# Performance work log

Measured on AMD Instinct MI355X. Metric: run time of the kernel, lower is better.

Reference implementation:

```python
import jax, jax.numpy as jnp
import numpy as np

N = 50000   # nodes
E = 800000  # edges (avg degree 16)
G = 256     # graphs in batch
H = 16      # hidden_channels
ADD = 7     # ADD_FEATURES
EPS = 1e-5


def setup_inputs() -> dict:
    key = jax.random.key(0)
    ks = jax.random.split(key, 32)
    inp = {
        "x": jax.random.normal(ks[0], (N, 1), dtype=jnp.float32),
        "edge_index": jax.random.randint(ks[1], (2, E), 0, N),
        "batch": jnp.sort(jax.random.randint(ks[2], (N,), 0, G)),
        "y_extra": jax.random.normal(ks[3], (G, ADD), dtype=jnp.float32),
    }
    k = 4
    conv_dims = [(1, H), (H, 2 * H), (2 * H, 4 * H), (4 * H, 8 * H)]
    for i, (ci, co) in enumerate(conv_dims, 1):
        inp[f"W{i}"] = (jax.random.normal(ks[k], (ci, co), dtype=jnp.float32) / np.float32(np.sqrt(ci))); k += 1
        inp[f"b{i}"] = jnp.zeros((co,), dtype=jnp.float32)
    for i, c in enumerate([H, 2 * H, 4 * H], 1):
        inp[f"g{i}"] = jnp.ones((c,), jnp.float32) + 0.1 * jax.random.normal(ks[k], (c,), dtype=jnp.float32); k += 1
        inp[f"be{i}"] = 0.1 * jax.random.normal(ks[k], (c,), dtype=jnp.float32); k += 1
    mlp_dims = [(8 * H + ADD, 128), (128, 64), (64, 32), (32, 2)]
    for i, (ci, co) in enumerate(mlp_dims, 1):
        inp[f"lw{i}"] = (jax.random.normal(ks[k], (ci, co), dtype=jnp.float32) / np.float32(np.sqrt(ci))); k += 1
        inp[f"lb{i}"] = 0.01 * jax.random.normal(ks[k], (co,), dtype=jnp.float32); k += 1
    return inp


def _gcn_norm(edge_index, n):
    # PyG GCNConv default: add self loops, symmetric deg^{-1/2} normalization.
    loops = jnp.arange(n)
    src = jnp.concatenate([edge_index[0], loops])
    dst = jnp.concatenate([edge_index[1], loops])
    deg = jax.ops.segment_sum(jnp.ones_like(src, dtype=jnp.float32), dst, num_segments=n)
    dis = jnp.where(deg > 0, jax.lax.rsqrt(jnp.maximum(deg, 1.0)), 0.0)
    return src, dst, dis[src] * dis[dst]


def _gcn_conv(x, W, b, src, dst, norm, n):
    h = x @ W                                   # [N, Cout]
    msg = h[src] * norm[:, None]                # [E+N, Cout] gather
    agg = jax.ops.segment_sum(msg, dst, num_segments=n)  # scatter-add
    return agg + b


def _bn(x, gamma, beta):
    # training-mode BatchNorm1d over node dim (biased variance)
    mu = jnp.mean(x, axis=0)
    var = jnp.mean(jnp.square(x - mu), axis=0)
    return gamma * (x - mu) * jax.lax.rsqrt(var + EPS) + beta


def _gelu(x):
    return jax.nn.gelu(x, approximate=False)  # torch F.gelu default = exact erf


def reference(x, edge_index, batch, y_extra,
              W1, b1, W2, b2, W3, b3, W4, b4,
              g1, be1, g2, be2, g3, be3,
              lw1, lb1, lw2, lb2, lw3, lb3, lw4, lb4):
    n = x.shape[0]
    src, dst, norm = _gcn_norm(edge_index, n)
    h = _gelu(_gcn_conv(x, W1, b1, src, dst, norm, n))
    h = _bn(h, g1, be1)
    h = _gelu(_gcn_conv(h, W2, b2, src, dst, norm, n))
    h = _bn(h, g2, be2)
    h = _gelu(_gcn_conv(h, W3, b3, src, dst, norm, n))
    h = _bn(h, g3, be3)
    h = _gelu(_gcn_conv(h, W4, b4, src, dst, norm, n))
    # global mean pool per graph
    sums = jax.ops.segment_sum(h, batch, num_segments=G)
    cnt = jax.ops.segment_sum(jnp.ones((n,), jnp.float32), batch, num_segments=G)
    pooled = sums / jnp.maximum(cnt, 1.0)[:, None]   # [G, 8H]
    z = jnp.concatenate([pooled, y_extra], axis=1)   # [G, 8H+7]
    z = _gelu(z @ lw1 + lb1)
    z = _gelu(z @ lw2 + lb2)
    z = _gelu(z @ lw3 + lb3)
    return jax.nn.sigmoid(z @ lw4 + lb4)             # [G, 2]
```

## Files before the change

### kernel.cpp

```cpp
#include <hip/hip_runtime.h>
#include <math.h>

#define NN 50000
#define EE 800000
#define GG 256
#define NPB 100
#define NBUCK 500
#define EPB 4096
#define NEB 196
#define NB_NODE 196

__device__ __forceinline__ float gelu_f(float v){
    return 0.5f * v * (1.0f + erff(v * 0.70710678118654752f));
}

__global__ __launch_bounds__(256) void k_hist(const int* __restrict__ dst, int* __restrict__ bucket_cnt_p, int e){
    __shared__ int hist[512];
    int t = threadIdx.x;
    int start = blockIdx.x * EPB;
    for (int k = t; k < 512; k += 256) hist[k] = 0;
    __syncthreads();
#pragma unroll
    for (int k = 0; k < EPB / 256; k++){
        int idx = start + k * 256 + t;
        if (idx < e) atomicAdd(&hist[dst[idx] / NPB], 1);
    }
    __syncthreads();
    for (int k = t; k < NBUCK; k += 256){
        int h = hist[k];
        if (h) atomicAdd(&bucket_cnt_p[k * 16], h);
    }
}

__global__ __launch_bounds__(512) void k_bscan(const int* __restrict__ bucket_cnt_p,
                                               int* __restrict__ bucket_off, int* __restrict__ cursor_p){
    __shared__ int s[512];
    int t = threadIdx.x;
    int v = (t < NBUCK) ? bucket_cnt_p[t * 16] : 0;
    s[t] = v;
    __syncthreads();
    for (int off = 1; off < 512; off <<= 1){
        int u = (t >= off) ? s[t - off] : 0;
        __syncthreads();
        s[t] += u;
        __syncthreads();
    }
    if (t < NBUCK){
        int ex = s[t] - v;
        bucket_off[t] = ex;
        cursor_p[t * 16] = ex;
    }
}

__global__ __launch_bounds__(256) void k_scatter(const int* __restrict__ src, const int* __restrict__ dst,
                                                 int* __restrict__ cursor_p, int* __restrict__ ebuf, int e){
    __shared__ int hist[512], base[512];
    int t = threadIdx.x;
    int start = blockIdx.x * EPB;
    for (int k = t; k < 512; k += 256) hist[k] = 0;
    __syncthreads();
    int pk[EPB / 256], bb[EPB / 256];
    int cntl = 0;
#pragma unroll
    for (int k = 0; k < EPB / 256; k++){
        int idx = start + k * 256 + t;
        if (idx < e){
            int s_ = src[idx], d_ = dst[idx];
            int b_ = d_ / NPB;
            pk[cntl] = (s_ << 7) | (d_ - b_ * NPB);
            bb[cntl] = b_;
            atomicAdd(&hist[b_], 1);
            cntl++;
        }
    }
    __syncthreads();
    for (int k = t; k < NBUCK; k += 256){
        int h = hist[k];
        base[k] = h ? atomicAdd(&cursor_p[k * 16], h) : 0;
    }
    __syncthreads();
    for (int k = t; k < 512; k += 256) hist[k] = 0;
    __syncthreads();
    for (int k = 0; k < cntl; k++){
        int b_ = bb[k];
        int pos = base[b_] + atomicAdd(&hist[b_], 1);
        ebuf[pos] = pk[k];
    }
}

__global__ __launch_bounds__(256) void k_build(const int* __restrict__ ebuf,
                                               const int* __restrict__ bucket_cnt_p,
                                               const int* __restrict__ bucket_off,
                                               int* __restrict__ rp, int* __restrict__ col,
                                               float* __restrict__ dis, float* __restrict__ invdis,
                                               float2* __restrict__ xd,
                                               const float* __restrict__ x, int n){
    int b = blockIdx.x;
    int t = threadIdx.x;
    int nbase = b * NPB;
    int eoff = bucket_off[b];
    int ecnt = bucket_cnt_p[b * 16];
    __shared__ int cnt[128], excl[128], cnt2[128], s[128];
    if (t < 128){ cnt[t] = 0; cnt2[t] = 0; }
    __syncthreads();
    for (int j = t; j < ecnt; j += 256)
        atomicAdd(&cnt[ebuf[eoff + j] & 127], 1);
    __syncthreads();
    int v = (t < 128) ? cnt[t] : 0;
    if (t < 128) s[t] = v;
    __syncthreads();
    for (int off = 1; off < 128; off <<= 1){
        int u = (t < 128 && t >= off) ? s[t - off] : 0;
        __syncthreads();
        if (t < 128) s[t] += u;
        __syncthreads();
    }
    if (t < 128) excl[t] = s[t] - v;
    __syncthreads();
    if (t < NPB){
        int node = nbase + t;
        int dgg = cnt[t];
        rp[node] = eoff + excl[t];
        float dv = rsqrtf((float)(dgg + 1));
        dis[node] = dv;
        invdis[node] = sqrtf((float)(dgg + 1));
        xd[node] = make_float2(dv * x[node], dv);
    }
    if (b == NBUCK - 1 && t == 0) rp[n] = eoff + ecnt;
    __syncthreads();
    for (int j = t; j < ecnt; j += 256){
        int v2 = ebuf[eoff + j];
        int li = v2 & 127;
        int p = eoff + excl[li] + atomicAdd(&cnt2[li], 1);
        col[p] = v2 >> 7;
    }
}

__global__ __launch_bounds__(256) void k_g1l1(const float2* __restrict__ xd,
                                              const int* __restrict__ rp, const int* __restrict__ col,
                                              const float* __restrict__ W, const float* __restrict__ bias,
                                              float* __restrict__ dsum, float* __restrict__ hs, int n){
    int node = blockIdx.x * 256 + threadIdx.x;
    if (node >= n) return;
    int beg = rp[node], end = rp[node + 1];
    float a0 = 0.f, a1 = 0.f, d0 = 0.f, d1 = 0.f;
    int j = beg;
    for (; j + 1 < end; j += 2){
        float2 v0 = xd[col[j]];
        float2 v1 = xd[col[j + 1]];
        a0 += v0.x; d0 += v0.y;
        a1 += v1.x; d1 += v1.y;
    }
    if (j < end){ float2 v0 = xd[col[j]]; a0 += v0.x; d0 += v0.y; }
    float2 self = xd[node];
    float dn = self.y;
    dsum[node] = d0 + d1 + dn;
    float a = dn * (a0 + a1 + self.x);
    float4* o = (float4*)(hs + (size_t)node * 16);
#pragma unroll
    for (int u = 0; u < 4; u++){
        float4 r;
        r.x = gelu_f(bias[u*4+0] + a * W[u*4+0]) * dn;
        r.y = gelu_f(bias[u*4+1] + a * W[u*4+1]) * dn;
        r.z = gelu_f(bias[u*4+2] + a * W[u*4+2]) * dn;
        r.w = gelu_f(bias[u*4+3] + a * W[u*4+3]) * dn;
        o[u] = r;
    }
}

template<int C>
__global__ __launch_bounds__(256) void k_gather(const float* __restrict__ hs, const int* __restrict__ rp,
                                                const int* __restrict__ col, const float* __restrict__ dis,
                                                const float* __restrict__ dsum, const float* __restrict__ stat,
                                                const float* __restrict__ gamma, const float* __restrict__ beta,
                                                float* __restrict__ outp, int n){
    constexpr int TPN = C / 4;
    int i = blockIdx.x * 256 + threadIdx.x;
    int node = i / TPN, q = i % TPN;
    if (node >= n) return;
    int c0 = q * 4;
    const float invn = 1.0f / (float)NN;
    float scv[4], shv[4];
#pragma unroll
    for (int u = 0; u < 4; u++){
        float mean = stat[c0 + u] * invn;
        float var  = stat[128 + c0 + u] * invn - mean * mean;
        float sc   = gamma[c0 + u] * rsqrtf(var + 1e-5f);
        scv[u] = sc;
        shv[u] = beta[c0 + u] - mean * sc;
    }
    const float4* h4 = (const float4*)hs;
    int beg = rp[node], end = rp[node + 1];
    float a0 = 0.f, a1 = 0.f, a2 = 0.f, a3 = 0.f;
    float b0 = 0.f, b1 = 0.f, b2 = 0.f, b3 = 0.f;
    int j = beg;
    for (; j + 7 < end; j += 8){
        int i0 = col[j],   i1 = col[j+1], i2 = col[j+2], i3 = col[j+3];
        int i4 = col[j+4], i5 = col[j+5], i6 = col[j+6], i7 = col[j+7];
        float4 v0 = h4[i0 * TPN + q];
        float4 v1 = h4[i1 * TPN + q];
        float4 v2 = h4[i2 * TPN + q];
        float4 v3 = h4[i3 * TPN + q];
        float4 v4 = h4[i4 * TPN + q];
        float4 v5 = h4[i5 * TPN + q];
        float4 v6 = h4[i6 * TPN + q];
        float4 v7 = h4[i7 * TPN + q];
        a0 += v0.x; a1 += v0.y; a2 += v0.z; a3 += v0.w;
        b0 += v1.x; b1 += v1.y; b2 += v1.z; b3 += v1.w;
        a0 += v2.x; a1 += v2.y; a2 += v2.z; a3 += v2.w;
        b0 += v3.x; b1 += v3.y; b2 += v3.z; b3 += v3.w;
        a0 += v4.x; a1 += v4.y; a2 += v4.z; a3 += v4.w;
        b0 += v5.x; b1 += v5.y; b2 += v5.z; b3 += v5.w;
        a0 += v6.x; a1 += v6.y; a2 += v6.z; a3 += v6.w;
        b0 += v7.x; b1 += v7.y; b2 += v7.z; b3 += v7.w;
    }
    for (; j < end; j++){
        float4 v = h4[col[j] * TPN + q];
        a0 += v.x; a1 += v.y; a2 += v.z; a3 += v.w;
    }
    float4 vs = h4[node * TPN + q];
    a0 += vs.x; a1 += vs.y; a2 += vs.z; a3 += vs.w;
    a0 += b0; a1 += b1; a2 += b2; a3 += b3;
    float dn = dis[node];
    float dsm = dsum[node];
    float4 r = make_float4((a0 * scv[0] + shv[0] * dsm) * dn,
                           (a1 * scv[1] + shv[1] * dsm) * dn,
                           (a2 * scv[2] + shv[2] * dsm) * dn,
                           (a3 * scv[3] + shv[3] * dsm) * dn);
    ((float4*)outp)[node * TPN + q] = r;
}

template<int CIN, int COUT, bool SCALE>
__global__ __launch_bounds__(256) void k_linT(const float* __restrict__ xin, const float* __restrict__ dis,
                                              const float* __restrict__ W,
                                              const float* __restrict__ bias, float* __restrict__ outp, int n){
    constexpr int QC = COUT / 4;
    constexpr int K4 = CIN / 4;
    int i = blockIdx.x * 256 + threadIdx.x;
    int tile = i / QC, q = i % QC;
    int n0 = tile * 4;
    if (n0 >= n) return;
    const float4* xp0 = (const float4*)(xin + (size_t)(n0 + 0) * CIN);
    const float4* xp1 = (const float4*)(xin + (size_t)(n0 + 1) * CIN);
    const float4* xp2 = (const float4*)(xin + (size_t)(n0 + 2) * CIN);
    const float4* xp3 = (const float4*)(xin + (size_t)(n0 + 3) * CIN);
    const float4* Wq = (const float4*)W + q;
    float4 bb = ((const float4*)bias)[q];
    float acc[4][4];
#pragma unroll
    for (int nd = 0; nd < 4; nd++){
        acc[nd][0] = bb.x; acc[nd][1] = bb.y; acc[nd][2] = bb.z; acc[nd][3] = bb.w;
    }
#pragma unroll 1
    for (int k4 = 0; k4 < K4; k4++){
        float4 xv[4];
        xv[0] = xp0[k4]; xv[1] = xp1[k4]; xv[2] = xp2[k4]; xv[3] = xp3[k4];
        float4 w0 = Wq[(k4 * 4 + 0) * QC];
        float4 w1 = Wq[(k4 * 4 + 1) * QC];
        float4 w2 = Wq[(k4 * 4 + 2) * QC];
        float4 w3 = Wq[(k4 * 4 + 3) * QC];
#pragma unroll
        for (int nd = 0; nd < 4; nd++){
            acc[nd][0] += xv[nd].x*w0.x + xv[nd].y*w1.x + xv[nd].z*w2.x + xv[nd].w*w3.x;
            acc[nd][1] += xv[nd].x*w0.y + xv[nd].y*w1.y + xv[nd].z*w2.y + xv[nd].w*w3.y;
            acc[nd][2] += xv[nd].x*w0.z + xv[nd].y*w1.z + xv[nd].z*w2.z + xv[nd].w*w3.z;
            acc[nd][3] += xv[nd].x*w0.w + xv[nd].y*w1.w + xv[nd].z*w2.w + xv[nd].w*w3.w;
        }
    }
    float4* o4 = (float4*)outp;
#pragma unroll
    for (int nd = 0; nd < 4; nd++){
        float sc = SCALE ? dis[n0 + nd] : 1.0f;
        o4[(size_t)(n0 + nd) * QC + q] =
            make_float4(gelu_f(acc[nd][0])*sc, gelu_f(acc[nd][1])*sc,
                        gelu_f(acc[nd][2])*sc, gelu_f(acc[nd][3])*sc);
    }
}

template<int C>
__global__ __launch_bounds__(256) void k_stats(const float* __restrict__ hs, const float* __restrict__ invdis,
                                               float* __restrict__ stat, int n){
    constexpr int REP = 256 / C;
    int t = threadIdx.x;
    int rep = t / C;
    int c = t % C;
    float s = 0.f, q = 0.f;
    for (int row = blockIdx.x * REP + rep; row < n; row += gridDim.x * REP){
        float v = hs[(long long)row * C + c] * invdis[row];
        s += v; q += v * v;
    }
    __shared__ float ss[256], sq[256];
    ss[t] = s; sq[t] = q;
    __syncthreads();
    for (int off = 128; off >= C; off >>= 1){
        if (t < off){ ss[t] += ss[t + off]; sq[t] += sq[t + off]; }
        __syncthreads();
    }
    if (t < C){
        atomicAdd(&stat[t], ss[t]);
        atomicAdd(&stat[128 + t], sq[t]);
    }
}

__global__ __launch_bounds__(128) void k_pool(const float* __restrict__ h4, const int* __restrict__ batch,
                                              float* __restrict__ pool, int n){
    int g = blockIdx.x;
    int t = threadIdx.x;
    int lo = 0, hi = n;
    while (lo < hi){ int mid = (lo + hi) >> 1; if (batch[mid] < g) lo = mid + 1; else hi = mid; }
    int s = lo;
    hi = n;
    while (lo < hi){ int mid = (lo + hi) >> 1; if (batch[mid] < g + 1) lo = mid + 1; else hi = mid; }
    int e = lo;
    float a0 = 0.f, a1 = 0.f, a2 = 0.f, a3 = 0.f;
    int node = s;
    for (; node + 3 < e; node += 4){
        a0 += h4[(size_t)(node + 0) * 128 + t];
        a1 += h4[(size_t)(node + 1) * 128 + t];
        a2 += h4[(size_t)(node + 2) * 128 + t];
        a3 += h4[(size_t)(node + 3) * 128 + t];
    }
    for (; node < e; node++) a0 += h4[(size_t)node * 128 + t];
    float sum = (a0 + a1) + (a2 + a3);
    pool[g * 128 + t] = sum / fmaxf((float)(e - s), 1.0f);
}

__global__ __launch_bounds__(128) void k_mlp(const float* __restrict__ pool,
                                             const float* __restrict__ yex,
                                             const float* __restrict__ lw1, const float* __restrict__ lb1,
                                             const float* __restrict__ lw2, const float* __restrict__ lb2,
                                             const float* __restrict__ lw3, const float* __restrict__ lb3,
                                             const float* __restrict__ lw4, const float* __restrict__ lb4,
                                             float* __restrict__ outp){
    int g = blockIdx.x;
    int t = threadIdx.x;
    __shared__ float z[136];
    __shared__ float z2[128];
    __shared__ float z3[64];
    __shared__ float z4[32];
    z[t] = pool[g * 128 + t];
    if (t < 7) z[128 + t] = yex[g * 7 + t];
    __syncthreads();
    {
        float acc = lb1[t];
        for (int k = 0; k < 135; k++) acc += z[k] * lw1[k * 128 + t];
        z2[t] = gelu_f(acc);
    }
    __syncthreads();
    if (t < 64){
        float acc = lb2[t];
        for (int k = 0; k < 128; k++) acc += z2[k] * lw2[k * 64 + t];
        z3[t] = gelu_f(acc);
    }
    __syncthreads();
    if (t < 32){
        float acc = lb3[t];
        for (int k = 0; k < 64; k++) acc += z3[k] * lw3[k * 32 + t];
        z4[t] = gelu_f(acc);
    }
    __syncthreads();
    if (t < 2){
        float acc = lb4[t];
        for (int k = 0; k < 32; k++) acc += z4[k] * lw4[k * 2 + t];
        outp[g * 2 + t] = 1.0f / (1.0f + expf(-acc));
    }
}

extern "C" void kernel_launch(void* const* d_in, const int* in_sizes, int n_in,
                              void* d_out, int out_size, void* d_ws, size_t ws_size,
                              hipStream_t stream) {
    const float* x     = (const float*)d_in[0];
    const int*   ei    = (const int*)  d_in[1];
    const int*   batch = (const int*)  d_in[2];
    const float* yex   = (const float*)d_in[3];
    const float* W1 = (const float*)d_in[4];  const float* b1 = (const float*)d_in[5];
    const float* W2 = (const float*)d_in[6];  const float* b2 = (const float*)d_in[7];
    const float* W3 = (const float*)d_in[8];  const float* b3 = (const float*)d_in[9];
    const float* W4 = (const float*)d_in[10]; const float* b4 = (const float*)d_in[11];
    const float* g1 = (const float*)d_in[12]; const float* be1 = (const float*)d_in[13];
    const float* g2 = (const float*)d_in[14]; const float* be2 = (const float*)d_in[15];
    const float* g3 = (const float*)d_in[16]; const float* be3 = (const float*)d_in[17];
    const float* lw1 = (const float*)d_in[18]; const float* lb1 = (const float*)d_in[19];
    const float* lw2 = (const float*)d_in[20]; const float* lb2 = (const float*)d_in[21];
    const float* lw3 = (const float*)d_in[22]; const float* lb3 = (const float*)d_in[23];
    const float* lw4 = (const float*)d_in[24]; const float* lb4 = (const float*)d_in[25];
    float* out = (float*)d_out;

    char* wsb = (char*)d_ws;
    size_t off = 0;
    auto alloc = [&](size_t elems) -> void* {
        void* p = wsb + off;
        off += ((elems * 4 + 255) / 256) * 256;
        return p;
    };
    float* stats        = (float*)alloc(3 * 256);
    int*   bucket_cnt_p = (int*)  alloc(NBUCK * 16);
    size_t zero_bytes = off;
    int*   bucket_off   = (int*)  alloc(NBUCK);
    int*   cursor_p     = (int*)  alloc(NBUCK * 16);
    int*   ebuf         = (int*)  alloc(EE);
    float* pool   = (float*)alloc(GG * 128);
    int*   rp     = (int*)  alloc(NN + 1);
    float* dis    = (float*)alloc(NN);
    float* invdis = (float*)alloc(NN);
    float* dsum   = (float*)alloc(NN);
    float2* xd    = (float2*)alloc(NN * 2);
    int*   col    = (int*)  alloc(EE);
    float* hbuf   = (float*)alloc((size_t)NN * 128);
    float* abuf   = (float*)alloc((size_t)NN * 64);

    hipMemsetAsync(d_ws, 0, zero_bytes, stream);

    auto nb = [](long long total){ return (int)((total + 255) / 256); };

    k_hist   <<<NEB, 256, 0, stream>>>(ei + EE, bucket_cnt_p, EE);
    k_bscan  <<<1, 512, 0, stream>>>(bucket_cnt_p, bucket_off, cursor_p);
    k_scatter<<<NEB, 256, 0, stream>>>(ei, ei + EE, cursor_p, ebuf, EE);
    k_build  <<<NBUCK, 256, 0, stream>>>(ebuf, bucket_cnt_p, bucket_off, rp, col, dis, invdis, xd, x, NN);

    k_g1l1<<<NB_NODE, 256, 0, stream>>>(xd, rp, col, W1, b1, dsum, hbuf, NN);
    k_stats<16><<<128, 256, 0, stream>>>(hbuf, invdis, stats + 0, NN);

    k_gather<16><<<nb((long long)NN * 4), 256, 0, stream>>>(hbuf, rp, col, dis, dsum, stats + 0, g1, be1, abuf, NN);
    k_linT<16, 32, true><<<nb((long long)(NN / 4) * 8), 256, 0, stream>>>(abuf, dis, W2, b2, hbuf, NN);
    k_stats<32><<<128, 256, 0, stream>>>(hbuf, invdis, stats + 256, NN);

    k_gather<32><<<nb((long long)NN * 8), 256, 0, stream>>>(hbuf, rp, col, dis, dsum, stats + 256, g2, be2, abuf, NN);
    k_linT<32, 64, true><<<nb((long long)(NN / 4) * 16), 256, 0, stream>>>(abuf, dis, W3, b3, hbuf, NN);
    k_stats<64><<<128, 256, 0, stream>>>(hbuf, invdis, stats + 512, NN);

    k_gather<64><<<nb((long long)NN * 16), 256, 0, stream>>>(hbuf, rp, col, dis, dsum, stats + 512, g3, be3, abuf, NN);
    k_linT<64, 128, false><<<nb((long long)(NN / 4) * 32), 256, 0, stream>>>(abuf, dis, W4, b4, hbuf, NN);
    k_pool<<<GG, 128, 0, stream>>>(hbuf, batch, pool, NN);

    k_mlp<<<GG, 128, 0, stream>>>(pool, yex,
                                  lw1, lb1, lw2, lb2, lw3, lb3, lw4, lb4, out);
}
```

Before: 363.0 us.

## Fuse neighbor gather with following linear layer via shared memory

Merges the per-layer gather+BN kernel and the dense linear+GELU kernel into one kernel per layer. Each block gathers aggregated, normalized features for its nodes into shared memory, loads the weight matrix into shared memory, then computes the linear transform from LDS. This removes the intermediate activation buffer's write and read to global memory and two launches per layer. It adds higher LDS usage (up to 32KB of weights for the last layer), which may reduce occupancy, and halves the threads per node in the gather.

```diff
diff --git a/kernel.cpp b/kernel.cpp
--- a/kernel.cpp
+++ b/kernel.cpp
@@ -168,97 +168,89 @@
     }
 }
 
-template<int C>
-__global__ __launch_bounds__(256) void k_gather(const float* __restrict__ hs, const int* __restrict__ rp,
-                                                const int* __restrict__ col, const float* __restrict__ dis,
-                                                const float* __restrict__ dsum, const float* __restrict__ stat,
-                                                const float* __restrict__ gamma, const float* __restrict__ beta,
-                                                float* __restrict__ outp, int n){
-    constexpr int TPN = C / 4;
-    int i = blockIdx.x * 256 + threadIdx.x;
-    int node = i / TPN, q = i % TPN;
-    if (node >= n) return;
-    int c0 = q * 4;
-    const float invn = 1.0f / (float)NN;
-    float scv[4], shv[4];
-#pragma unroll
-    for (int u = 0; u < 4; u++){
-        float mean = stat[c0 + u] * invn;
-        float var  = stat[128 + c0 + u] * invn - mean * mean;
-        float sc   = gamma[c0 + u] * rsqrtf(var + 1e-5f);
-        scv[u] = sc;
-        shv[u] = beta[c0 + u] - mean * sc;
-    }
-    const float4* h4 = (const float4*)hs;
-    int beg = rp[node], end = rp[node + 1];
-    float a0 = 0.f, a1 = 0.f, a2 = 0.f, a3 = 0.f;
-    float b0 = 0.f, b1 = 0.f, b2 = 0.f, b3 = 0.f;
-    int j = beg;
-    for (; j + 7 < end; j += 8){
-        int i0 = col[j],   i1 = col[j+1], i2 = col[j+2], i3 = col[j+3];
-        int i4 = col[j+4], i5 = col[j+5], i6 = col[j+6], i7 = col[j+7];
-        float4 v0 = h4[i0 * TPN + q];
-        float4 v1 = h4[i1 * TPN + q];
-        float4 v2 = h4[i2 * TPN + q];
-        float4 v3 = h4[i3 * TPN + q];
-        float4 v4 = h4[i4 * TPN + q];
-        float4 v5 = h4[i5 * TPN + q];
-        float4 v6 = h4[i6 * TPN + q];
-        float4 v7 = h4[i7 * TPN + q];
-        a0 += v0.x; a1 += v0.y; a2 += v0.z; a3 += v0.w;
-        b0 += v1.x; b1 += v1.y; b2 += v1.z; b3 += v1.w;
-        a0 += v2.x; a1 += v2.y; a2 += v2.z; a3 += v2.w;
-        b0 += v3.x; b1 += v3.y; b2 += v3.z; b3 += v3.w;
-        a0 += v4.x; a1 += v4.y; a2 += v4.z; a3 += v4.w;
-        b0 += v5.x; b1 += v5.y; b2 += v5.z; b3 += v5.w;
-        a0 += v6.x; a1 += v6.y; a2 += v6.z; a3 += v6.w;
-        b0 += v7.x; b1 += v7.y; b2 += v7.z; b3 += v7.w;
-    }
-    for (; j < end; j++){
-        float4 v = h4[col[j] * TPN + q];
-        a0 += v.x; a1 += v.y; a2 += v.z; a3 += v.w;
-    }
-    float4 vs = h4[node * TPN + q];
-    a0 += vs.x; a1 += vs.y; a2 += vs.z; a3 += vs.w;
-    a0 += b0; a1 += b1; a2 += b2; a3 += b3;
-    float dn = dis[node];
-    float dsm = dsum[node];
-    float4 r = make_float4((a0 * scv[0] + shv[0] * dsm) * dn,
-                           (a1 * scv[1] + shv[1] * dsm) * dn,
-                           (a2 * scv[2] + shv[2] * dsm) * dn,
-                           (a3 * scv[3] + shv[3] * dsm) * dn);
-    ((float4*)outp)[node * TPN + q] = r;
-}
-
 template<int CIN, int COUT, bool SCALE>
-__global__ __launch_bounds__(256) void k_linT(const float* __restrict__ xin, const float* __restrict__ dis,
-                                              const float* __restrict__ W,
-                                              const float* __restrict__ bias, float* __restrict__ outp, int n){
-    constexpr int QC = COUT / 4;
-    constexpr int K4 = CIN / 4;
-    int i = blockIdx.x * 256 + threadIdx.x;
-    int tile = i / QC, q = i % QC;
-    int n0 = tile * 4;
-    if (n0 >= n) return;
-    const float4* xp0 = (const float4*)(xin + (size_t)(n0 + 0) * CIN);
-    const float4* xp1 = (const float4*)(xin + (size_t)(n0 + 1) * CIN);
-    const float4* xp2 = (const float4*)(xin + (size_t)(n0 + 2) * CIN);
-    const float4* xp3 = (const float4*)(xin + (size_t)(n0 + 3) * CIN);
-    const float4* Wq = (const float4*)W + q;
-    float4 bb = ((const float4*)bias)[q];
+__global__ __launch_bounds__(256) void k_gl(const float* __restrict__ hs_in, const int* __restrict__ rp,
+                                            const int* __restrict__ col, const float* __restrict__ dis,
+                                            const float* __restrict__ dsum, const float* __restrict__ stat,
+                                            const float* __restrict__ gamma, const float* __restrict__ beta,
+                                            const float* __restrict__ W, const float* __restrict__ bias,
+                                            float* __restrict__ hs_out, int n){
+    constexpr int TPN = CIN / 8;
+    constexpr int NB  = 256 / TPN;
+    constexpr int KF  = CIN / 4;
+    constexpr int QF  = COUT / 4;
+    __shared__ float4 WL[CIN * QF];
+    __shared__ float4 aL[NB * KF];
+    int t = threadIdx.x;
+    for (int idx = t; idx < CIN * QF; idx += 256)
+        WL[idx] = ((const float4*)W)[idx];
+
+    int nl = t / TPN, q8 = t % TPN;
+    int q2 = q8 * 2;
+    int node = blockIdx.x * NB + nl;
+    if (node < n){
+        int c0 = q8 * 8;
+        const float invn = 1.0f / (float)NN;
+        float scv[8], shv[8];
+#pragma unroll
+        for (int u = 0; u < 8; u++){
+            float mean = stat[c0 + u] * invn;
+            float var  = stat[128 + c0 + u] * invn - mean * mean;
+            float sc   = gamma[c0 + u] * rsqrtf(var + 1e-5f);
+            scv[u] = sc;
+            shv[u] = beta[c0 + u] - mean * sc;
+        }
+        const float4* h4 = (const float4*)hs_in;
+        int beg = rp[node], end = rp[node + 1];
+        float sa0=0.f,sa1=0.f,sa2=0.f,sa3=0.f, sb0=0.f,sb1=0.f,sb2=0.f,sb3=0.f;
+        int j = beg;
+        for (; j + 3 < end; j += 4){
+            int i0 = col[j], i1 = col[j+1], i2 = col[j+2], i3 = col[j+3];
+            float4 va0 = h4[i0 * KF + q2], vb0 = h4[i0 * KF + q2 + 1];
+            float4 va1 = h4[i1 * KF + q2], vb1 = h4[i1 * KF + q2 + 1];
+            float4 va2 = h4[i2 * KF + q2], vb2 = h4[i2 * KF + q2 + 1];
+            float4 va3 = h4[i3 * KF + q2], vb3 = h4[i3 * KF + q2 + 1];
+            sa0 += va0.x + va2.x; sa1 += va0.y + va2.y; sa2 += va0.z + va2.z; sa3 += va0.w + va2.w;
+            sb0 += vb0.x + vb2.x; sb1 += vb0.y + vb2.y; sb2 += vb0.z + vb2.z; sb3 += vb0.w + vb2.w;
+            sa0 += va1.x + va3.x; sa1 += va1.y + va3.y; sa2 += va1.z + va3.z; sa3 += va1.w + va3.w;
+            sb0 += vb1.x + vb3.x; sb1 += vb1.y + vb3.y; sb2 += vb1.z + vb3.z; sb3 += vb1.w + vb3.w;
+        }
+        for (; j < end; j++){
+            int i0 = col[j];
+            float4 va = h4[i0 * KF + q2], vb = h4[i0 * KF + q2 + 1];
+            sa0 += va.x; sa1 += va.y; sa2 += va.z; sa3 += va.w;
+            sb0 += vb.x; sb1 += vb.y; sb2 += vb.z; sb3 += vb.w;
+        }
+        float4 vsa = h4[node * KF + q2], vsb = h4[node * KF + q2 + 1];
+        sa0 += vsa.x; sa1 += vsa.y; sa2 += vsa.z; sa3 += vsa.w;
+        sb0 += vsb.x; sb1 += vsb.y; sb2 += vsb.z; sb3 += vsb.w;
+        float dn  = dis[node];
+        float dsm = dsum[node];
+        aL[nl * KF + q2]     = make_float4((sa0*scv[0]+shv[0]*dsm)*dn, (sa1*scv[1]+shv[1]*dsm)*dn,
+                                           (sa2*scv[2]+shv[2]*dsm)*dn, (sa3*scv[3]+shv[3]*dsm)*dn);
+        aL[nl * KF + q2 + 1] = make_float4((sb0*scv[4]+shv[4]*dsm)*dn, (sb1*scv[5]+shv[5]*dsm)*dn,
+                                           (sb2*scv[6]+shv[6]*dsm)*dn, (sb3*scv[7]+shv[7]*dsm)*dn);
+    }
+    __syncthreads();
+
+    int ng = t / QF, qg = t % QF;
+    int n0l = ng * 4;
+    int n0 = blockIdx.x * NB + n0l;
+    float4 bb = ((const float4*)bias)[qg];
     float acc[4][4];
 #pragma unroll
     for (int nd = 0; nd < 4; nd++){
         acc[nd][0] = bb.x; acc[nd][1] = bb.y; acc[nd][2] = bb.z; acc[nd][3] = bb.w;
     }
 #pragma unroll 1
-    for (int k4 = 0; k4 < K4; k4++){
+    for (int k4 = 0; k4 < KF; k4++){
         float4 xv[4];
-        xv[0] = xp0[k4]; xv[1] = xp1[k4]; xv[2] = xp2[k4]; xv[3] = xp3[k4];
-        float4 w0 = Wq[(k4 * 4 + 0) * QC];
-        float4 w1 = Wq[(k4 * 4 + 1) * QC];
-        float4 w2 = Wq[(k4 * 4 + 2) * QC];
-        float4 w3 = Wq[(k4 * 4 + 3) * QC];
+#pragma unroll
+        for (int nd = 0; nd < 4; nd++) xv[nd] = aL[(n0l + nd) * KF + k4];
+        float4 w0 = WL[(k4 * 4 + 0) * QF + qg];
+        float4 w1 = WL[(k4 * 4 + 1) * QF + qg];
+        float4 w2 = WL[(k4 * 4 + 2) * QF + qg];
+        float4 w3 = WL[(k4 * 4 + 3) * QF + qg];
 #pragma unroll
         for (int nd = 0; nd < 4; nd++){
             acc[nd][0] += xv[nd].x*w0.x + xv[nd].y*w1.x + xv[nd].z*w2.x + xv[nd].w*w3.x;
@@ -267,13 +259,16 @@
             acc[nd][3] += xv[nd].x*w0.w + xv[nd].y*w1.w + xv[nd].z*w2.w + xv[nd].w*w3.w;
         }
     }
-    float4* o4 = (float4*)outp;
+    float4* o4 = (float4*)hs_out;
 #pragma unroll
     for (int nd = 0; nd < 4; nd++){
-        float sc = SCALE ? dis[n0 + nd] : 1.0f;
-        o4[(size_t)(n0 + nd) * QC + q] =
-            make_float4(gelu_f(acc[nd][0])*sc, gelu_f(acc[nd][1])*sc,
-                        gelu_f(acc[nd][2])*sc, gelu_f(acc[nd][3])*sc);
+        int onode = n0 + nd;
+        if (onode < n){
+            float sc = SCALE ? dis[onode] : 1.0f;
+            o4[(size_t)onode * QF + qg] =
+                make_float4(gelu_f(acc[nd][0])*sc, gelu_f(acc[nd][1])*sc,
+                            gelu_f(acc[nd][2])*sc, gelu_f(acc[nd][3])*sc);
+        }
     }
 }
 
@@ -406,32 +401,30 @@
     float* dsum   = (float*)alloc(NN);
     float2* xd    = (float2*)alloc(NN * 2);
     int*   col    = (int*)  alloc(EE);
-    float* hbuf   = (float*)alloc((size_t)NN * 128);
-    float* abuf   = (float*)alloc((size_t)NN * 64);
+    float* hbufA  = (float*)alloc((size_t)NN * 64);
+    float* hbufB  = (float*)alloc((size_t)NN * 128);
 
     hipMemsetAsync(d_ws, 0, zero_bytes, stream);
-
-    auto nb = [](long long total){ return (int)((total + 255) / 256); };
 
     k_hist   <<<NEB, 256, 0, stream>>>(ei + EE, bucket_cnt_p, EE);
     k_bscan  <<<1, 512, 0, stream>>>(bucket_cnt_p, bucket_off, cursor_p);
     k_scatter<<<NEB, 256, 0, stream>>>(ei, ei + EE, cursor_p, ebuf, EE);
     k_build  <<<NBUCK, 256, 0, stream>>>(ebuf, bucket_cnt_p, bucket_off, rp, col, dis, invdis, xd, x, NN);
 
-    k_g1l1<<<NB_NODE, 256, 0, stream>>>(xd, rp, col, W1, b1, dsum, hbuf, NN);
-    k_stats<16><<<128, 256, 0, stream>>>(hbuf, invdis, stats + 0, NN);
-
-    k_gather<16><<<nb((long long)NN * 4), 256, 0, stream>>>(hbuf, rp, col, dis, dsum, stats + 0, g1, be1, abuf, NN);
-    k_linT<16, 32, true><<<nb((long long)(NN / 4) * 8), 256, 0, stream>>>(abuf, dis, W2, b2, hbuf, NN);
-    k_stats<32><<<128, 256, 0, stream>>>(hbuf, invdis, stats + 256, NN);
-
-    k_gather<32><<<nb((long long)NN * 8), 256, 0, stream>>>(hbuf, rp, col, dis, dsum, stats + 256, g2, be2, abuf, NN);
-    k_linT<32, 64, true><<<nb((long long)(NN / 4) * 16), 256, 0, stream>>>(abuf, dis, W3, b3, hbuf, NN);
-    k_stats<64><<<128, 256, 0, stream>>>(hbuf, invdis, stats + 512, NN);
-
-    k_gather<64><<<nb((long long)NN * 16), 256, 0, stream>>>(hbuf, rp, col, dis, dsum, stats + 512, g3, be3, abuf, NN);
-    k_linT<64, 128, false><<<nb((long long)(NN / 4) * 32), 256, 0, stream>>>(abuf, dis, W4, b4, hbuf, NN);
-    k_pool<<<GG, 128, 0, stream>>>(hbuf, batch, pool, NN);
+    k_g1l1<<<NB_NODE, 256, 0, stream>>>(xd, rp, col, W1, b1, dsum, hbufA, NN);
+    k_stats<16><<<128, 256, 0, stream>>>(hbufA, invdis, stats + 0, NN);
+
+    k_gl<16, 32, true><<<(NN + 127) / 128, 256, 0, stream>>>(hbufA, rp, col, dis, dsum, stats + 0,
+                                                             g1, be1, W2, b2, hbufB, NN);
+    k_stats<32><<<128, 256, 0, stream>>>(hbufB, invdis, stats + 256, NN);
+
+    k_gl<32, 64, true><<<(NN + 63) / 64, 256, 0, stream>>>(hbufB, rp, col, dis, dsum, stats + 256,
+                                                           g2, be2, W3, b3, hbufA, NN);
+    k_stats<64><<<128, 256, 0, stream>>>(hbufA, invdis, stats + 512, NN);
+
+    k_gl<64, 128, false><<<(NN + 31) / 32, 256, 0, stream>>>(hbufA, rp, col, dis, dsum, stats + 512,
+                                                             g3, be3, W4, b4, hbufB, NN);
+    k_pool<<<GG, 128, 0, stream>>>(hbufB, batch, pool, NN);
 
     k_mlp<<<GG, 128, 0, stream>>>(pool, yex,
                                   lw1, lb1, lw2, lb2, lw3, lb3, lw4, lb4, out);
```

Result: faster. 330.2 us (-9.0%).
